# Performance work log

Hardware: AMD Instinct MI355X
Metric: run time of the kernel (lower is better)

The kernel has to match this reference:

```python
import jax, jax.numpy as jnp
import numpy as np

OUT, IN = 4096, 4096
BLOCK = 32
NBLK = IN // BLOCK  # 128


def setup_inputs() -> dict:
    key = jax.random.key(0)
    k1, k2, k3 = jax.random.split(key, 3)
    x = jax.random.normal(k1, (2, 2048, IN), dtype=jnp.float32)
    # per-block scales (GGUF stores fp16 scales; small magnitude typical)
    scales = jax.random.normal(k2, (OUT, NBLK), dtype=jnp.float32) * 0.01
    # int8 codes stored as unsigned 0..255; signed value = code - 128
    codes = jax.random.randint(k3, (OUT, NBLK, BLOCK), 0, 256, dtype=jnp.int32)
    return {"x": x, "scales": scales, "codes": codes}


def dequantize_q8_0(scales, codes):
    # scales: [out, nblk], codes: [out, nblk, 32] unsigned -> signed int8 semantics
    signed = codes.astype(jnp.float32) - 128.0
    w = scales[:, :, None] * signed            # [out, nblk, 32]
    return w.reshape(OUT, IN)                   # [out, in]


def reference(x, scales, codes):
    weight = dequantize_q8_0(scales, codes)     # [out, in]
    # nn.functional.linear: y = x @ weight.T
    return jnp.einsum("bsi,oi->bso", x, weight)
```

## Files before the change

kernel.cpp:

```cpp
#include <hip/hip_runtime.h>
#include <hip/hip_bf16.h>
#include <stdint.h>


#define M_DIM 4096
#define N_DIM 4096
#define K_DIM 4096
#define TILE 128
#define BK 32

typedef __attribute__((ext_vector_type(8))) short bf16x8;
typedef __attribute__((ext_vector_type(4))) float f32x4;

__device__ __forceinline__ unsigned short f32_to_bf16_rne(float f) {
    unsigned u = __float_as_uint(f);
    u += 0x7fffu + ((u >> 16) & 1u);
    return (unsigned short)(u >> 16);
}

__device__ __forceinline__ void load_lds16(const void* g, void* l) {
    __builtin_amdgcn_global_load_lds(
        (const __attribute__((address_space(1))) unsigned int*)g,
        (__attribute__((address_space(3))) unsigned int*)l, 16, 0, 0);
}

__global__ __launch_bounds__(256) void dequant_w_kernel(
        const int* __restrict__ codes, const float* __restrict__ scales,
        unsigned short* __restrict__ W) {
    const int tid = blockIdx.x * 256 + threadIdx.x;
    const int o   = tid >> 9;
    const int blk = (tid & 511) >> 2;
    const float s = scales[o * 128 + blk];
    const int4 c0 = ((const int4*)codes)[(size_t)tid * 2];
    const int4 c1 = ((const int4*)codes)[(size_t)tid * 2 + 1];
    union { unsigned short u[8]; uint4 v; } p;
    p.u[0] = f32_to_bf16_rne(s * (float)(c0.x - 128));
    p.u[1] = f32_to_bf16_rne(s * (float)(c0.y - 128));
    p.u[2] = f32_to_bf16_rne(s * (float)(c0.z - 128));
    p.u[3] = f32_to_bf16_rne(s * (float)(c0.w - 128));
    p.u[4] = f32_to_bf16_rne(s * (float)(c1.x - 128));
    p.u[5] = f32_to_bf16_rne(s * (float)(c1.y - 128));
    p.u[6] = f32_to_bf16_rne(s * (float)(c1.z - 128));
    p.u[7] = f32_to_bf16_rne(s * (float)(c1.w - 128));
    ((uint4*)W)[tid] = p.v;
}

__global__ __launch_bounds__(256) void cvt_x_kernel(
        const float* __restrict__ x, unsigned short* __restrict__ xb) {
    const int tid = blockIdx.x * 256 + threadIdx.x;
    const float4 f0 = ((const float4*)x)[(size_t)tid * 2];
    const float4 f1 = ((const float4*)x)[(size_t)tid * 2 + 1];
    union { unsigned short u[8]; uint4 v; } p;
    p.u[0] = f32_to_bf16_rne(f0.x); p.u[1] = f32_to_bf16_rne(f0.y);
    p.u[2] = f32_to_bf16_rne(f0.z); p.u[3] = f32_to_bf16_rne(f0.w);
    p.u[4] = f32_to_bf16_rne(f1.x); p.u[5] = f32_to_bf16_rne(f1.y);
    p.u[6] = f32_to_bf16_rne(f1.z); p.u[7] = f32_to_bf16_rne(f1.w);
    ((uint4*)xb)[tid] = p.v;
}

__global__ __launch_bounds__(256) void gemm_bt_kernel(
        const unsigned short* __restrict__ A,
        const unsigned short* __restrict__ B,
        float* __restrict__ C) {
    __shared__ unsigned short As[TILE * BK];
    __shared__ unsigned short Bs[TILE * BK];

    const int wave = threadIdx.x >> 6;
    const int lane = threadIdx.x & 63;
    const int m0 = blockIdx.y * TILE;
    const int n0 = blockIdx.x * TILE;

    const int srow  = lane >> 2;
    const int skofs = (lane & 3) * 8;
    const int wrow0 = wave * 32;

    const unsigned short* Ag = A + (size_t)(m0 + wrow0 + srow) * K_DIM + skofs;
    const unsigned short* Bg = B + (size_t)(n0 + wrow0 + srow) * K_DIM + skofs;
    unsigned short* AsBase = &As[wrow0 * BK];
    unsigned short* BsBase = &Bs[wrow0 * BK];

    const int frow = lane & 15;
    const int quad = lane >> 4;
    const int wm = (wave >> 1) * 64;
    const int wn = (wave & 1) * 64;

    f32x4 acc[4][4] = {};

    for (int k0 = 0; k0 < K_DIM; k0 += BK) {
        load_lds16(Ag + k0,               AsBase);
        load_lds16(Ag + k0 + 16 * K_DIM,  AsBase + 16 * BK);
        load_lds16(Bg + k0,               BsBase);
        load_lds16(Bg + k0 + 16 * K_DIM,  BsBase + 16 * BK);
        __syncthreads();

        bf16x8 a[4], b[4];
#pragma unroll
        for (int t = 0; t < 4; ++t) {
            a[t] = *(const bf16x8*)&As[(wm + t * 16 + frow) * BK + quad * 8];
            b[t] = *(const bf16x8*)&Bs[(wn + t * 16 + frow) * BK + quad * 8];
        }
#pragma unroll
        for (int mt = 0; mt < 4; ++mt)
#pragma unroll
            for (int nt = 0; nt < 4; ++nt)
                acc[mt][nt] = __builtin_amdgcn_mfma_f32_16x16x32_bf16(
                    a[mt], b[nt], acc[mt][nt], 0, 0, 0);
        __syncthreads();
    }

#pragma unroll
    for (int mt = 0; mt < 4; ++mt)
#pragma unroll
        for (int nt = 0; nt < 4; ++nt)
#pragma unroll
            for (int r = 0; r < 4; ++r) {
                const int row = m0 + wm + mt * 16 + quad * 4 + r;
                const int col = n0 + wn + nt * 16 + frow;
                C[(size_t)row * N_DIM + col] = acc[mt][nt][r];
            }
}

extern "C" void kernel_launch(void* const* d_in, const int* in_sizes, int n_in,
                              void* d_out, int out_size, void* d_ws, size_t ws_size,
                              hipStream_t stream) {
    const float* x      = (const float*)d_in[0];
    const float* scales = (const float*)d_in[1];
    const int*   codes  = (const int*)d_in[2];
    float* y = (float*)d_out;

    unsigned short* Wb = (unsigned short*)d_ws;
    unsigned short* xb = (unsigned short*)((char*)d_ws + (size_t)N_DIM * K_DIM * 2);

    dequant_w_kernel<<<8192, 256, 0, stream>>>(codes, scales, Wb);
    cvt_x_kernel<<<8192, 256, 0, stream>>>(x, xb);

    dim3 grid(N_DIM / TILE, M_DIM / TILE);
    gemm_bt_kernel<<<grid, 256, 0, stream>>>(xb, Wb, y);
}
```

Measured before the change: 353.6 us.

## Double GEMM K-tile with XOR-swizzled LDS, remap block order, merge prologue kernels

Doubles the K tile to 64 so each barrier pair covers twice the MFMA work, and XOR-swizzles the LDS column chunks on both the global-to-LDS copy and the fragment reads to avoid bank conflicts. The GEMM grid becomes 1D with a remapped tile order, likely to spread tiles across XCDs and improve L2 locality. The dequant and x-convert kernels are merged into one launch to save a launch and a gap between kernels. The cost is doubled LDS use per block, which may lower occupancy.

```diff
diff --git a/kernel.cpp b/kernel.cpp
--- a/kernel.cpp
+++ b/kernel.cpp
@@ -7,7 +7,7 @@
 #define N_DIM 4096
 #define K_DIM 4096
 #define TILE 128
-#define BK 32
+#define BK 64
 
 typedef __attribute__((ext_vector_type(8))) short bf16x8;
 typedef __attribute__((ext_vector_type(4))) float f32x4;
@@ -24,38 +24,39 @@
         (__attribute__((address_space(3))) unsigned int*)l, 16, 0, 0);
 }
 
-__global__ __launch_bounds__(256) void dequant_w_kernel(
+__global__ __launch_bounds__(256) void prologue_kernel(
         const int* __restrict__ codes, const float* __restrict__ scales,
-        unsigned short* __restrict__ W) {
-    const int tid = blockIdx.x * 256 + threadIdx.x;
-    const int o   = tid >> 9;
-    const int blk = (tid & 511) >> 2;
-    const float s = scales[o * 128 + blk];
-    const int4 c0 = ((const int4*)codes)[(size_t)tid * 2];
-    const int4 c1 = ((const int4*)codes)[(size_t)tid * 2 + 1];
-    union { unsigned short u[8]; uint4 v; } p;
-    p.u[0] = f32_to_bf16_rne(s * (float)(c0.x - 128));
-    p.u[1] = f32_to_bf16_rne(s * (float)(c0.y - 128));
-    p.u[2] = f32_to_bf16_rne(s * (float)(c0.z - 128));
-    p.u[3] = f32_to_bf16_rne(s * (float)(c0.w - 128));
-    p.u[4] = f32_to_bf16_rne(s * (float)(c1.x - 128));
-    p.u[5] = f32_to_bf16_rne(s * (float)(c1.y - 128));
-    p.u[6] = f32_to_bf16_rne(s * (float)(c1.z - 128));
-    p.u[7] = f32_to_bf16_rne(s * (float)(c1.w - 128));
-    ((uint4*)W)[tid] = p.v;
-}
-
-__global__ __launch_bounds__(256) void cvt_x_kernel(
+        unsigned short* __restrict__ W,
         const float* __restrict__ x, unsigned short* __restrict__ xb) {
-    const int tid = blockIdx.x * 256 + threadIdx.x;
-    const float4 f0 = ((const float4*)x)[(size_t)tid * 2];
-    const float4 f1 = ((const float4*)x)[(size_t)tid * 2 + 1];
-    union { unsigned short u[8]; uint4 v; } p;
-    p.u[0] = f32_to_bf16_rne(f0.x); p.u[1] = f32_to_bf16_rne(f0.y);
-    p.u[2] = f32_to_bf16_rne(f0.z); p.u[3] = f32_to_bf16_rne(f0.w);
-    p.u[4] = f32_to_bf16_rne(f1.x); p.u[5] = f32_to_bf16_rne(f1.y);
-    p.u[6] = f32_to_bf16_rne(f1.z); p.u[7] = f32_to_bf16_rne(f1.w);
-    ((uint4*)xb)[tid] = p.v;
+    const int bid = blockIdx.x;
+    if (bid < 8192) {
+        const int tid = bid * 256 + threadIdx.x;
+        const int o   = tid >> 9;
+        const int blk = (tid & 511) >> 2;
+        const float s = scales[o * 128 + blk];
+        const int4 c0 = ((const int4*)codes)[(size_t)tid * 2];
+        const int4 c1 = ((const int4*)codes)[(size_t)tid * 2 + 1];
+        union { unsigned short u[8]; uint4 v; } p;
+        p.u[0] = f32_to_bf16_rne(s * (float)(c0.x - 128));
+        p.u[1] = f32_to_bf16_rne(s * (float)(c0.y - 128));
+        p.u[2] = f32_to_bf16_rne(s * (float)(c0.z - 128));
+        p.u[3] = f32_to_bf16_rne(s * (float)(c0.w - 128));
+        p.u[4] = f32_to_bf16_rne(s * (float)(c1.x - 128));
+        p.u[5] = f32_to_bf16_rne(s * (float)(c1.y - 128));
+        p.u[6] = f32_to_bf16_rne(s * (float)(c1.z - 128));
+        p.u[7] = f32_to_bf16_rne(s * (float)(c1.w - 128));
+        ((uint4*)W)[tid] = p.v;
+    } else {
+        const int tid = (bid - 8192) * 256 + threadIdx.x;
+        const float4 f0 = ((const float4*)x)[(size_t)tid * 2];
+        const float4 f1 = ((const float4*)x)[(size_t)tid * 2 + 1];
+        union { unsigned short u[8]; uint4 v; } p;
+        p.u[0] = f32_to_bf16_rne(f0.x); p.u[1] = f32_to_bf16_rne(f0.y);
+        p.u[2] = f32_to_bf16_rne(f0.z); p.u[3] = f32_to_bf16_rne(f0.w);
+        p.u[4] = f32_to_bf16_rne(f1.x); p.u[5] = f32_to_bf16_rne(f1.y);
+        p.u[6] = f32_to_bf16_rne(f1.z); p.u[7] = f32_to_bf16_rne(f1.w);
+        ((uint4*)xb)[tid] = p.v;
+    }
 }
 
 __global__ __launch_bounds__(256) void gemm_bt_kernel(
@@ -67,11 +68,16 @@
 
     const int wave = threadIdx.x >> 6;
     const int lane = threadIdx.x & 63;
-    const int m0 = blockIdx.y * TILE;
-    const int n0 = blockIdx.x * TILE;
 
-    const int srow  = lane >> 2;
-    const int skofs = (lane & 3) * 8;
+    const int b   = blockIdx.x;
+    const int i   = b >> 3;
+    const int mt0 = ((b >> 2) & 1) * 16 + (i & 15);
+    const int nt0 = (b & 3) * 8 + (i >> 4);
+    const int m0 = mt0 * TILE;
+    const int n0 = nt0 * TILE;
+
+    const int srow  = lane >> 3;
+    const int skofs = ((lane & 7) ^ srow) * 8;
     const int wrow0 = wave * 32;
 
     const unsigned short* Ag = A + (size_t)(m0 + wrow0 + srow) * K_DIM + skofs;
@@ -87,24 +93,31 @@
     f32x4 acc[4][4] = {};
 
     for (int k0 = 0; k0 < K_DIM; k0 += BK) {
-        load_lds16(Ag + k0,               AsBase);
-        load_lds16(Ag + k0 + 16 * K_DIM,  AsBase + 16 * BK);
-        load_lds16(Bg + k0,               BsBase);
-        load_lds16(Bg + k0 + 16 * K_DIM,  BsBase + 16 * BK);
+#pragma unroll
+        for (int j = 0; j < 4; ++j) {
+            load_lds16(Ag + k0 + j * 8 * K_DIM, AsBase + j * 8 * BK);
+            load_lds16(Bg + k0 + j * 8 * K_DIM, BsBase + j * 8 * BK);
+        }
         __syncthreads();
 
-        bf16x8 a[4], b[4];
 #pragma unroll
-        for (int t = 0; t < 4; ++t) {
-            a[t] = *(const bf16x8*)&As[(wm + t * 16 + frow) * BK + quad * 8];
-            b[t] = *(const bf16x8*)&Bs[(wn + t * 16 + frow) * BK + quad * 8];
+        for (int h = 0; h < 2; ++h) {
+            bf16x8 a[4], bfr[4];
+#pragma unroll
+            for (int t = 0; t < 4; ++t) {
+                const int ar = wm + t * 16 + frow;
+                const int br = wn + t * 16 + frow;
+                const int ch = (h * 4 + quad) ^ (frow & 7);
+                a[t]   = *(const bf16x8*)&As[ar * BK + ch * 8];
+                bfr[t] = *(const bf16x8*)&Bs[br * BK + ch * 8];
+            }
+#pragma unroll
+            for (int mt = 0; mt < 4; ++mt)
+#pragma unroll
+                for (int nt = 0; nt < 4; ++nt)
+                    acc[mt][nt] = __builtin_amdgcn_mfma_f32_16x16x32_bf16(
+                        a[mt], bfr[nt], acc[mt][nt], 0, 0, 0);
         }
-#pragma unroll
-        for (int mt = 0; mt < 4; ++mt)
-#pragma unroll
-            for (int nt = 0; nt < 4; ++nt)
-                acc[mt][nt] = __builtin_amdgcn_mfma_f32_16x16x32_bf16(
-                    a[mt], b[nt], acc[mt][nt], 0, 0, 0);
         __syncthreads();
     }
 
@@ -131,9 +144,7 @@
     unsigned short* Wb = (unsigned short*)d_ws;
     unsigned short* xb = (unsigned short*)((char*)d_ws + (size_t)N_DIM * K_DIM * 2);
 
-    dequant_w_kernel<<<8192, 256, 0, stream>>>(codes, scales, Wb);
-    cvt_x_kernel<<<8192, 256, 0, stream>>>(x, xb);
+    prologue_kernel<<<16384, 256, 0, stream>>>(codes, scales, Wb, x, xb);
 
-    dim3 grid(N_DIM / TILE, M_DIM / TILE);
-    gemm_bt_kernel<<<grid, 256, 0, stream>>>(xb, Wb, y);
+    gemm_bt_kernel<<<1024, 256, 0, stream>>>(xb, Wb, y);
 }
```

New measurement: 317.0 us. 10.3% less time.
